# Kernel optimization log

Measured on AMD Instinct MI355X. Metric: run time of the kernel, lower is better.

The kernel has to match this reference:

```python
import jax, jax.numpy as jnp
import numpy as np

BS, SL, ENC_DIM, EDGE_DIM = 8, 256, 1024, 256
MINUS_INF = -1.0e8


def setup_inputs() -> dict:
    key = jax.random.key(0)
    ks = jax.random.split(key, 5)
    encoded_text = jax.random.normal(ks[0], (BS, SL, ENC_DIM), dtype=jnp.float32)
    mask = jnp.ones((BS, SL), dtype=jnp.int64)
    # Linear params (torch stores weight as (out, in)); scale like default init
    Wh = jax.random.normal(ks[1], (EDGE_DIM, ENC_DIM), dtype=jnp.float32) / np.sqrt(ENC_DIM)
    bh = jax.random.normal(ks[2], (EDGE_DIM,), dtype=jnp.float32) / np.sqrt(ENC_DIM)
    Wc = jax.random.normal(ks[3], (EDGE_DIM, ENC_DIM), dtype=jnp.float32) / np.sqrt(ENC_DIM)
    w_out = jax.random.normal(ks[4], (EDGE_DIM,), dtype=jnp.float32) / np.sqrt(EDGE_DIM)
    return {"encoded_text": encoded_text, "mask": mask, "Wh": Wh, "bh": bh, "Wc": Wc, "w_out": w_out}


def reference(encoded_text, mask, Wh, bh, Wc, w_out):
    # head/child projections: (bs, sl, edge_dim)
    head = jnp.einsum('bse,de->bsd', encoded_text, Wh) + bh
    child = jnp.einsum('bse,de->bsd', encoded_text, Wc)
    # Pairwise: torch code gives combined[b,i,j] = tanh(head[b,j] + child[b,i])
    combined = jnp.tanh(head[:, None, :, :] + child[:, :, None, :])  # (bs, sl, sl, edge_dim)
    edge_scores = jnp.einsum('bijd,d->bij', combined, w_out)  # (bs, sl, sl)
    float_mask = mask.astype(jnp.float32)
    minus_mask = (1.0 - float_mask) * MINUS_INF  # (bs, sl)
    edge_scores = edge_scores + minus_mask[:, :, None] + minus_mask[:, None, :]
    return edge_scores
```

## Files before the change

### kernel.cpp

```cpp
#include <hip/hip_runtime.h>
#include <hip/hip_bf16.h>
#include <stdint.h>


typedef __bf16 bf16_t;
typedef __attribute__((ext_vector_type(8))) __bf16 bf16x8;
typedef __attribute__((ext_vector_type(4))) float f32x4;

#define SL 256
#define ENC 1024
#define NTOT 512
#define N_ENC 2097152
#define N_W 262144
#define KSCALE 2.8853900817779268f

__device__ __forceinline__ void async16(void* lds, const void* g) {
  __builtin_amdgcn_global_load_lds(
      (const __attribute__((address_space(1))) uint32_t*)g,
      (__attribute__((address_space(3))) uint32_t*)lds, 16, 0, 0);
}
__device__ __forceinline__ unsigned short f32_to_bf16_rne(float f) {
  uint32_t u = __float_as_uint(f);
  return (unsigned short)((u + 0x7FFFu + ((u >> 16) & 1u)) >> 16);
}
__device__ __forceinline__ float bfu(unsigned short h) {
  return __uint_as_float(((uint32_t)h) << 16);
}

__global__ __launch_bounds__(256)
void convert_kernel(const float* __restrict__ enc, const float* __restrict__ Wh,
                    const float* __restrict__ Wc,
                    unsigned short* __restrict__ encB, unsigned short* __restrict__ WB) {
  int gi = (blockIdx.x * 256 + threadIdx.x) * 4;
  const float* src;
  unsigned short* dst;
  int off;
  if (gi < N_ENC) {
    src = enc; off = gi; dst = encB + gi;
  } else if (gi < N_ENC + N_W) {
    src = Wh; off = gi - N_ENC; dst = WB + off;
  } else {
    src = Wc; off = gi - N_ENC - N_W; dst = WB + N_W + off;
  }
  f32x4 v = *(const f32x4*)(src + off);
  ushort4 o;
  o.x = f32_to_bf16_rne(v[0]); o.y = f32_to_bf16_rne(v[1]);
  o.z = f32_to_bf16_rne(v[2]); o.w = f32_to_bf16_rne(v[3]);
  *(ushort4*)dst = o;
}

__global__ void prep_kernel(const float* __restrict__ bh, const float* __restrict__ wout,
                            const int* __restrict__ mask,
                            float* __restrict__ bhF, float* __restrict__ w2F,
                            float* __restrict__ Ssum, float* __restrict__ mmF) {
  int t = threadIdx.x;
  bhF[t] = bh[t];
  float w = wout[t];
  w2F[t] = -2.0f * w;
  __shared__ float red[256];
  red[t] = w;
  __syncthreads();
  for (int s = 128; s > 0; s >>= 1) {
    if (t < s) red[t] += red[t + s];
    __syncthreads();
  }
  if (t == 0) Ssum[0] = red[0];
  for (int s = t; s < 2048; s += 256)
    mmF[s] = (1.0f - (float)mask[s]) * -1.0e8f;
}

__global__ __launch_bounds__(256)
void proj_kernel(const unsigned short* __restrict__ A, const unsigned short* __restrict__ WB,
                 const float* __restrict__ bhF, float* __restrict__ hc) {
  __shared__ bf16_t As[64 * 32];
  __shared__ bf16_t Bs[64 * 32];
  const int t = threadIdx.x;
  const int wv = t >> 6, lane = t & 63;
  const int m0 = blockIdx.x * 64;
  const int n0 = blockIdx.y * 64;
  const int srow = t >> 2, schunk = t & 3;
  const int mq = (wv & 1) * 32, nq = (wv >> 1) * 32;
  const int fr = lane & 15, kq = lane >> 4;

  f32x4 acc00 = {0.f, 0.f, 0.f, 0.f};
  f32x4 acc01 = acc00, acc10 = acc00, acc11 = acc00;

  const unsigned short* gA = A + (size_t)(m0 + srow) * ENC + schunk * 8;
  const unsigned short* gB = WB + (size_t)(n0 + srow) * ENC + schunk * 8;

  for (int k0 = 0; k0 < ENC; k0 += 32) {
    __syncthreads();
    async16(&As[wv * 512], gA + k0);
    async16(&Bs[wv * 512], gB + k0);
    __syncthreads();
    bf16x8 a0 = *(const bf16x8*)&As[(mq + fr) * 32 + kq * 8];
    bf16x8 a1 = *(const bf16x8*)&As[(mq + 16 + fr) * 32 + kq * 8];
    bf16x8 b0 = *(const bf16x8*)&Bs[(nq + fr) * 32 + kq * 8];
    bf16x8 b1 = *(const bf16x8*)&Bs[(nq + 16 + fr) * 32 + kq * 8];
    acc00 = __builtin_amdgcn_mfma_f32_16x16x32_bf16(a0, b0, acc00, 0, 0, 0);
    acc01 = __builtin_amdgcn_mfma_f32_16x16x32_bf16(a0, b1, acc01, 0, 0, 0);
    acc10 = __builtin_amdgcn_mfma_f32_16x16x32_bf16(a1, b0, acc10, 0, 0, 0);
    acc11 = __builtin_amdgcn_mfma_f32_16x16x32_bf16(a1, b1, acc11, 0, 0, 0);
  }
  const int colA = n0 + nq + fr;
  const int colB = colA + 16;
  const float biasA = (colA < 256) ? bhF[colA] : 0.0f;
  const float biasB = (colB < 256) ? bhF[colB] : 0.0f;
#pragma unroll
  for (int r = 0; r < 4; ++r) {
    int row0 = m0 + mq + kq * 4 + r;
    int row1 = row0 + 16;
    hc[(size_t)row0 * NTOT + colA] = KSCALE * (acc00[r] + biasA);
    hc[(size_t)row0 * NTOT + colB] = KSCALE * (acc01[r] + biasB);
    hc[(size_t)row1 * NTOT + colA] = KSCALE * (acc10[r] + biasA);
    hc[(size_t)row1 * NTOT + colB] = KSCALE * (acc11[r] + biasB);
  }
}

#define LSTR 260
__global__ __launch_bounds__(256)
void edge_kernel(const float* __restrict__ hc, const float* __restrict__ w2,
                 const float* __restrict__ Ssum, const float* __restrict__ mmF,
                 float* __restrict__ out) {
  __shared__ float ldH[32 * LSTR];
  __shared__ float ldC[32 * LSTR];
  const int t = threadIdx.x;
  const int b = blockIdx.z;
  const int i0 = blockIdx.y * 32;
  const int j0 = blockIdx.x * 32;
  const int sbase = b * SL;

  for (int u = t; u < 32 * 64; u += 256) {
    int row = u >> 6;
    int c4 = (u & 63) << 2;
    f32x4 hv = *(const f32x4*)&hc[(size_t)(sbase + j0 + row) * NTOT + c4];
    f32x4 cv = *(const f32x4*)&hc[(size_t)(sbase + i0 + row) * NTOT + 256 + c4];
    *(f32x4*)&ldH[row * LSTR + c4] = hv;
    *(f32x4*)&ldC[row * LSTR + c4] = cv;
  }
  __syncthreads();

  const float S = Ssum[0];
  const int tx = t & 15, ty = t >> 4;
  const float* hp0 = &ldH[tx * LSTR];
  const float* hp1 = &ldH[(tx + 16) * LSTR];
  const float* cp0 = &ldC[ty * LSTR];
  const float* cp1 = &ldC[(ty + 16) * LSTR];
  float a00 = 0.f, a01 = 0.f, a10 = 0.f, a11 = 0.f;

#pragma unroll 8
  for (int d = 0; d < 256; d += 4) {
    f32x4 h0 = *(const f32x4*)&hp0[d];
    f32x4 h1 = *(const f32x4*)&hp1[d];
    f32x4 c0 = *(const f32x4*)&cp0[d];
    f32x4 c1 = *(const f32x4*)&cp1[d];
    f32x4 w4 = *(const f32x4*)&w2[d];
#pragma unroll
    for (int e = 0; e < 4; ++e) {
      float he0 = h0[e], he1 = h1[e], ce0 = c0[e], ce1 = c1[e], we = w4[e];
      float r00 = __builtin_amdgcn_rcpf(__builtin_amdgcn_exp2f(ce0 + he0) + 1.0f);
      float r01 = __builtin_amdgcn_rcpf(__builtin_amdgcn_exp2f(ce0 + he1) + 1.0f);
      float r10 = __builtin_amdgcn_rcpf(__builtin_amdgcn_exp2f(ce1 + he0) + 1.0f);
      float r11 = __builtin_amdgcn_rcpf(__builtin_amdgcn_exp2f(ce1 + he1) + 1.0f);
      a00 = fmaf(we, r00, a00);
      a01 = fmaf(we, r01, a01);
      a10 = fmaf(we, r10, a10);
      a11 = fmaf(we, r11, a11);
    }
  }

  const int gi0 = sbase + i0 + ty, gi1 = gi0 + 16;
  const int gj0 = j0 + tx, gj1 = gj0 + 16;
  const float mi0 = mmF[gi0], mi1 = mmF[gi1];
  const float mj0 = mmF[sbase + gj0], mj1 = mmF[sbase + gj1];
  out[(size_t)gi0 * SL + gj0] = S + a00 + mi0 + mj0;
  out[(size_t)gi0 * SL + gj1] = S + a01 + mi0 + mj1;
  out[(size_t)gi1 * SL + gj0] = S + a10 + mi1 + mj0;
  out[(size_t)gi1 * SL + gj1] = S + a11 + mi1 + mj1;
}

#define ED 256
#define HSTR 264
__global__ __launch_bounds__(256)
void kgedges_f32out(const float* __restrict__ enc, const int* __restrict__ mask,
                    const float* __restrict__ Wh, const float* __restrict__ Wc,
                    const float* __restrict__ p3, const float* __restrict__ p5,
                    float* __restrict__ out) {
  __shared__ float Wt[64 * 64];
  __shared__ float Et[32 * 64];
  __shared__ unsigned short headS[32 * HSTR];
  __shared__ unsigned short childS[32 * HSTR];
  __shared__ float red[256];
  __shared__ float bhS[256];
  __shared__ float wS[256];
  const int t = threadIdx.x;
  const int j0 = blockIdx.x * 32, i0 = blockIdx.y * 32, b = blockIdx.z;
  float va = p3[t], vb = p5[t];
  red[t] = va * va;
  __syncthreads();
  for (int s = 128; s > 0; s >>= 1) { if (t < s) red[t] += red[t + s]; __syncthreads(); }
  const float sa = red[0];
  __syncthreads();
  red[t] = vb * vb;
  __syncthreads();
  for (int s = 128; s > 0; s >>= 1) { if (t < s) red[t] += red[t + s]; __syncthreads(); }
  const float sb = red[0];
  __syncthreads();
  const bool dictOrder = (sa <= sb);
  bhS[t] = dictOrder ? va : vb;
  wS[t] = dictOrder ? vb : va;
  const int g = t >> 3;
  const int e = t & 7;
  for (int ph = 0; ph < 2; ++ph) {
    const float* Wsrc = ph ? Wc : Wh;
    const int rbase = b * SL + (ph ? i0 : j0);
    unsigned short* dst = ph ? childS : headS;
    for (int d0 = 0; d0 < ED; d0 += 64) {
      float acc[8] = {0.f, 0.f, 0.f, 0.f, 0.f, 0.f, 0.f, 0.f};
      for (int k0 = 0; k0 < ENC; k0 += 64) {
        __syncthreads();
#pragma unroll
        for (int p = 0; p < 4; ++p) {
          int u = t + 256 * p;
          int r = u >> 4, c4 = (u & 15) << 2;
          *(f32x4*)&Wt[r * 64 + c4] =
              *(const f32x4*)&Wsrc[(size_t)(d0 + r) * ENC + k0 + c4];
        }
#pragma unroll
        for (int p = 0; p < 2; ++p) {
          int u = t + 256 * p;
          int r = u >> 4, c4 = (u & 15) << 2;
          *(f32x4*)&Et[r * 64 + c4] =
              *(const f32x4*)&enc[(size_t)(rbase + r) * ENC + k0 + c4];
        }
        __syncthreads();
        for (int k4 = 0; k4 < 64; k4 += 4) {
          f32x4 ev = *(const f32x4*)&Et[g * 64 + k4];
#pragma unroll
          for (int m = 0; m < 8; ++m) {
            f32x4 wv = *(const f32x4*)&Wt[(e + 8 * m) * 64 + k4];
            acc[m] = fmaf(ev[0], wv[0], acc[m]);
            acc[m] = fmaf(ev[1], wv[1], acc[m]);
            acc[m] = fmaf(ev[2], wv[2], acc[m]);
            acc[m] = fmaf(ev[3], wv[3], acc[m]);
          }
        }
      }
#pragma unroll
      for (int m = 0; m < 8; ++m) {
        int d = d0 + e + 8 * m;
        float v = acc[m] + (ph == 0 ? bhS[d] : 0.0f);
        dst[g * HSTR + d] = f32_to_bf16_rne(v);
      }
    }
  }
  __syncthreads();
#pragma unroll
  for (int rep = 0; rep < 4; ++rep) {
    int idx = t + 256 * rep;
    int ii = idx >> 5, jj = idx & 31;
    float a = 0.f;
    for (int d = 0; d < ED; ++d) {
      float hv = bfu(headS[jj * HSTR + d]);
      float cv = bfu(childS[ii * HSTR + d]);
      a = fmaf(wS[d], tanhf(hv + cv), a);
    }
    int gi = b * SL + i0 + ii;
    int gj = j0 + jj;
    float mi = (1.0f - (float)mask[gi]) * -1.0e8f;
    float mj = (1.0f - (float)mask[b * SL + gj]) * -1.0e8f;
    out[(size_t)gi * SL + gj] = a + mi + mj;
  }
}

extern "C" void kernel_launch(void* const* d_in, const int* in_sizes, int n_in,
                              void* d_out, int out_size, void* d_ws, size_t ws_size,
                              hipStream_t stream) {
  (void)in_sizes; (void)n_in; (void)out_size;
  const float* enc = (const float*)d_in[0];
  const int* mask = (const int*)d_in[1];
  const float* Wh = (const float*)d_in[2];
  const float* bh = (const float*)d_in[3];
  const float* Wc = (const float*)d_in[4];
  const float* wout = (const float*)d_in[5];
  float* out = (float*)d_out;

  const size_t NEED = (size_t)(9u << 20) + (512u << 10);
  if (ws_size >= NEED) {
    char* W = (char*)d_ws;
    float* hc = (float*)W;
    unsigned short* encB = (unsigned short*)(W + (4 << 20));
    unsigned short* WB = (unsigned short*)(W + (8 << 20));
    float* bhF = (float*)(W + (9 << 20));
    float* w2F = bhF + 256;
    float* Ssum = w2F + 256;
    float* mmF = Ssum + 16;
    convert_kernel<<<2560, 256, 0, stream>>>(enc, Wh, Wc, encB, WB);
    prep_kernel<<<1, 256, 0, stream>>>(bh, wout, mask, bhF, w2F, Ssum, mmF);
    proj_kernel<<<dim3(32, 8), 256, 0, stream>>>(encB, WB, bhF, hc);
    edge_kernel<<<dim3(8, 8, 8), 256, 0, stream>>>(hc, w2F, Ssum, mmF, out);
  } else {
    kgedges_f32out<<<dim3(8, 8, 8), 256, 0, stream>>>(enc, mask, Wh, Wc, bh, wout, out);
  }
}
```

Baseline: 115.9 us.

## Precompute exp2 of projections and fold prep kernel into edge kernel

The projection epilogue now stores exp2 of the scaled head/child values, so the pairwise inner loop computes exp(h+c) as a product and drops one transcendental per element. The separate prep kernel is removed: the edge kernel reduces w_out into shared memory and computes the mask offsets itself, saving a launch. The fused fallback kernel and the workspace-size check are also removed. Storing exponentials risks overflow or underflow to inf/0 for large projection values, though the rcp form still saturates toward ±1 for tanh.

```diff
diff --git a/kernel.cpp b/kernel.cpp
--- a/kernel.cpp
+++ b/kernel.cpp
@@ -23,9 +23,6 @@
   uint32_t u = __float_as_uint(f);
   return (unsigned short)((u + 0x7FFFu + ((u >> 16) & 1u)) >> 16);
 }
-__device__ __forceinline__ float bfu(unsigned short h) {
-  return __uint_as_float(((uint32_t)h) << 16);
-}
 
 __global__ __launch_bounds__(256)
 void convert_kernel(const float* __restrict__ enc, const float* __restrict__ Wh,
@@ -49,29 +46,9 @@
   *(ushort4*)dst = o;
 }
 
-__global__ void prep_kernel(const float* __restrict__ bh, const float* __restrict__ wout,
-                            const int* __restrict__ mask,
-                            float* __restrict__ bhF, float* __restrict__ w2F,
-                            float* __restrict__ Ssum, float* __restrict__ mmF) {
-  int t = threadIdx.x;
-  bhF[t] = bh[t];
-  float w = wout[t];
-  w2F[t] = -2.0f * w;
-  __shared__ float red[256];
-  red[t] = w;
-  __syncthreads();
-  for (int s = 128; s > 0; s >>= 1) {
-    if (t < s) red[t] += red[t + s];
-    __syncthreads();
-  }
-  if (t == 0) Ssum[0] = red[0];
-  for (int s = t; s < 2048; s += 256)
-    mmF[s] = (1.0f - (float)mask[s]) * -1.0e8f;
-}
-
 __global__ __launch_bounds__(256)
 void proj_kernel(const unsigned short* __restrict__ A, const unsigned short* __restrict__ WB,
-                 const float* __restrict__ bhF, float* __restrict__ hc) {
+                 const float* __restrict__ bh, float* __restrict__ hc) {
   __shared__ bf16_t As[64 * 32];
   __shared__ bf16_t Bs[64 * 32];
   const int t = threadIdx.x;
@@ -104,31 +81,36 @@
   }
   const int colA = n0 + nq + fr;
   const int colB = colA + 16;
-  const float biasA = (colA < 256) ? bhF[colA] : 0.0f;
-  const float biasB = (colB < 256) ? bhF[colB] : 0.0f;
+  const float biasA = (colA < 256) ? bh[colA] : 0.0f;
+  const float biasB = (colB < 256) ? bh[colB] : 0.0f;
 #pragma unroll
   for (int r = 0; r < 4; ++r) {
     int row0 = m0 + mq + kq * 4 + r;
     int row1 = row0 + 16;
-    hc[(size_t)row0 * NTOT + colA] = KSCALE * (acc00[r] + biasA);
-    hc[(size_t)row0 * NTOT + colB] = KSCALE * (acc01[r] + biasB);
-    hc[(size_t)row1 * NTOT + colA] = KSCALE * (acc10[r] + biasA);
-    hc[(size_t)row1 * NTOT + colB] = KSCALE * (acc11[r] + biasB);
+    hc[(size_t)row0 * NTOT + colA] = __builtin_amdgcn_exp2f(KSCALE * (acc00[r] + biasA));
+    hc[(size_t)row0 * NTOT + colB] = __builtin_amdgcn_exp2f(KSCALE * (acc01[r] + biasB));
+    hc[(size_t)row1 * NTOT + colA] = __builtin_amdgcn_exp2f(KSCALE * (acc10[r] + biasA));
+    hc[(size_t)row1 * NTOT + colB] = __builtin_amdgcn_exp2f(KSCALE * (acc11[r] + biasB));
   }
 }
 
 #define LSTR 260
 __global__ __launch_bounds__(256)
-void edge_kernel(const float* __restrict__ hc, const float* __restrict__ w2,
-                 const float* __restrict__ Ssum, const float* __restrict__ mmF,
-                 float* __restrict__ out) {
+void edge_kernel(const float* __restrict__ hc, const float* __restrict__ wout,
+                 const int* __restrict__ mask, float* __restrict__ out) {
   __shared__ float ldH[32 * LSTR];
   __shared__ float ldC[32 * LSTR];
+  __shared__ float wS[256];
+  __shared__ float red[256];
   const int t = threadIdx.x;
   const int b = blockIdx.z;
   const int i0 = blockIdx.y * 32;
   const int j0 = blockIdx.x * 32;
   const int sbase = b * SL;
+
+  float w = wout[t];
+  wS[t] = -2.0f * w;
+  red[t] = w;
 
   for (int u = t; u < 32 * 64; u += 256) {
     int row = u >> 6;
@@ -139,8 +121,12 @@
     *(f32x4*)&ldC[row * LSTR + c4] = cv;
   }
   __syncthreads();
+  for (int s = 128; s > 0; s >>= 1) {
+    if (t < s) red[t] += red[t + s];
+    __syncthreads();
+  }
+  const float S = red[0];
 
-  const float S = Ssum[0];
   const int tx = t & 15, ty = t >> 4;
   const float* hp0 = &ldH[tx * LSTR];
   const float* hp1 = &ldH[(tx + 16) * LSTR];
@@ -154,14 +140,14 @@
     f32x4 h1 = *(const f32x4*)&hp1[d];
     f32x4 c0 = *(const f32x4*)&cp0[d];
     f32x4 c1 = *(const f32x4*)&cp1[d];
-    f32x4 w4 = *(const f32x4*)&w2[d];
+    f32x4 w4 = *(const f32x4*)&wS[d];
 #pragma unroll
     for (int e = 0; e < 4; ++e) {
       float he0 = h0[e], he1 = h1[e], ce0 = c0[e], ce1 = c1[e], we = w4[e];
-      float r00 = __builtin_amdgcn_rcpf(__builtin_amdgcn_exp2f(ce0 + he0) + 1.0f);
-      float r01 = __builtin_amdgcn_rcpf(__builtin_amdgcn_exp2f(ce0 + he1) + 1.0f);
-      float r10 = __builtin_amdgcn_rcpf(__builtin_amdgcn_exp2f(ce1 + he0) + 1.0f);
-      float r11 = __builtin_amdgcn_rcpf(__builtin_amdgcn_exp2f(ce1 + he1) + 1.0f);
+      float r00 = __builtin_amdgcn_rcpf(ce0 * he0 + 1.0f);
+      float r01 = __builtin_amdgcn_rcpf(ce0 * he1 + 1.0f);
+      float r10 = __builtin_amdgcn_rcpf(ce1 * he0 + 1.0f);
+      float r11 = __builtin_amdgcn_rcpf(ce1 * he1 + 1.0f);
       a00 = fmaf(we, r00, a00);
       a01 = fmaf(we, r01, a01);
       a10 = fmaf(we, r10, a10);
@@ -171,112 +157,20 @@
 
   const int gi0 = sbase + i0 + ty, gi1 = gi0 + 16;
   const int gj0 = j0 + tx, gj1 = gj0 + 16;
-  const float mi0 = mmF[gi0], mi1 = mmF[gi1];
-  const float mj0 = mmF[sbase + gj0], mj1 = mmF[sbase + gj1];
+  const float mi0 = (1.0f - (float)mask[gi0]) * -1.0e8f;
+  const float mi1 = (1.0f - (float)mask[gi1]) * -1.0e8f;
+  const float mj0 = (1.0f - (float)mask[sbase + gj0]) * -1.0e8f;
+  const float mj1 = (1.0f - (float)mask[sbase + gj1]) * -1.0e8f;
   out[(size_t)gi0 * SL + gj0] = S + a00 + mi0 + mj0;
   out[(size_t)gi0 * SL + gj1] = S + a01 + mi0 + mj1;
   out[(size_t)gi1 * SL + gj0] = S + a10 + mi1 + mj0;
   out[(size_t)gi1 * SL + gj1] = S + a11 + mi1 + mj1;
 }
 
-#define ED 256
-#define HSTR 264
-__global__ __launch_bounds__(256)
-void kgedges_f32out(const float* __restrict__ enc, const int* __restrict__ mask,
-                    const float* __restrict__ Wh, const float* __restrict__ Wc,
-                    const float* __restrict__ p3, const float* __restrict__ p5,
-                    float* __restrict__ out) {
-  __shared__ float Wt[64 * 64];
-  __shared__ float Et[32 * 64];
-  __shared__ unsigned short headS[32 * HSTR];
-  __shared__ unsigned short childS[32 * HSTR];
-  __shared__ float red[256];
-  __shared__ float bhS[256];
-  __shared__ float wS[256];
-  const int t = threadIdx.x;
-  const int j0 = blockIdx.x * 32, i0 = blockIdx.y * 32, b = blockIdx.z;
-  float va = p3[t], vb = p5[t];
-  red[t] = va * va;
-  __syncthreads();
-  for (int s = 128; s > 0; s >>= 1) { if (t < s) red[t] += red[t + s]; __syncthreads(); }
-  const float sa = red[0];
-  __syncthreads();
-  red[t] = vb * vb;
-  __syncthreads();
-  for (int s = 128; s > 0; s >>= 1) { if (t < s) red[t] += red[t + s]; __syncthreads(); }
-  const float sb = red[0];
-  __syncthreads();
-  const bool dictOrder = (sa <= sb);
-  bhS[t] = dictOrder ? va : vb;
-  wS[t] = dictOrder ? vb : va;
-  const int g = t >> 3;
-  const int e = t & 7;
-  for (int ph = 0; ph < 2; ++ph) {
-    const float* Wsrc = ph ? Wc : Wh;
-    const int rbase = b * SL + (ph ? i0 : j0);
-    unsigned short* dst = ph ? childS : headS;
-    for (int d0 = 0; d0 < ED; d0 += 64) {
-      float acc[8] = {0.f, 0.f, 0.f, 0.f, 0.f, 0.f, 0.f, 0.f};
-      for (int k0 = 0; k0 < ENC; k0 += 64) {
-        __syncthreads();
-#pragma unroll
-        for (int p = 0; p < 4; ++p) {
-          int u = t + 256 * p;
-          int r = u >> 4, c4 = (u & 15) << 2;
-          *(f32x4*)&Wt[r * 64 + c4] =
-              *(const f32x4*)&Wsrc[(size_t)(d0 + r) * ENC + k0 + c4];
-        }
-#pragma unroll
-        for (int p = 0; p < 2; ++p) {
-          int u = t + 256 * p;
-          int r = u >> 4, c4 = (u & 15) << 2;
-          *(f32x4*)&Et[r * 64 + c4] =
-              *(const f32x4*)&enc[(size_t)(rbase + r) * ENC + k0 + c4];
-        }
-        __syncthreads();
-        for (int k4 = 0; k4 < 64; k4 += 4) {
-          f32x4 ev = *(const f32x4*)&Et[g * 64 + k4];
-#pragma unroll
-          for (int m = 0; m < 8; ++m) {
-            f32x4 wv = *(const f32x4*)&Wt[(e + 8 * m) * 64 + k4];
-            acc[m] = fmaf(ev[0], wv[0], acc[m]);
-            acc[m] = fmaf(ev[1], wv[1], acc[m]);
-            acc[m] = fmaf(ev[2], wv[2], acc[m]);
-            acc[m] = fmaf(ev[3], wv[3], acc[m]);
-          }
-        }
-      }
-#pragma unroll
-      for (int m = 0; m < 8; ++m) {
-        int d = d0 + e + 8 * m;
-        float v = acc[m] + (ph == 0 ? bhS[d] : 0.0f);
-        dst[g * HSTR + d] = f32_to_bf16_rne(v);
-      }
-    }
-  }
-  __syncthreads();
-#pragma unroll
-  for (int rep = 0; rep < 4; ++rep) {
-    int idx = t + 256 * rep;
-    int ii = idx >> 5, jj = idx & 31;
-    float a = 0.f;
-    for (int d = 0; d < ED; ++d) {
-      float hv = bfu(headS[jj * HSTR + d]);
-      float cv = bfu(childS[ii * HSTR + d]);
-      a = fmaf(wS[d], tanhf(hv + cv), a);
-    }
-    int gi = b * SL + i0 + ii;
-    int gj = j0 + jj;
-    float mi = (1.0f - (float)mask[gi]) * -1.0e8f;
-    float mj = (1.0f - (float)mask[b * SL + gj]) * -1.0e8f;
-    out[(size_t)gi * SL + gj] = a + mi + mj;
-  }
-}
-
 extern "C" void kernel_launch(void* const* d_in, const int* in_sizes, int n_in,
                               void* d_out, int out_size, void* d_ws, size_t ws_size,
                               hipStream_t stream) {
-  (void)in_sizes; (void)n_in; (void)out_size;
+  (void)in_sizes; (void)n_in; (void)out_size; (void)ws_size;
   const float* enc = (const float*)d_in[0];
   const int* mask = (const int*)d_in[1];
   const float* Wh = (const float*)d_in[2];
@@ -285,21 +179,12 @@
   const float* wout = (const float*)d_in[5];
   float* out = (float*)d_out;
 
-  const size_t NEED = (size_t)(9u << 20) + (512u << 10);
-  if (ws_size >= NEED) {
-    char* W = (char*)d_ws;
-    float* hc = (float*)W;
-    unsigned short* encB = (unsigned short*)(W + (4 << 20));
-    unsigned short* WB = (unsigned short*)(W + (8 << 20));
-    float* bhF = (float*)(W + (9 << 20));
-    float* w2F = bhF + 256;
-    float* Ssum = w2F + 256;
-    float* mmF = Ssum + 16;
-    convert_kernel<<<2560, 256, 0, stream>>>(enc, Wh, Wc, encB, WB);
-    prep_kernel<<<1, 256, 0, stream>>>(bh, wout, mask, bhF, w2F, Ssum, mmF);
-    proj_kernel<<<dim3(32, 8), 256, 0, stream>>>(encB, WB, bhF, hc);
-    edge_kernel<<<dim3(8, 8, 8), 256, 0, stream>>>(hc, w2F, Ssum, mmF, out);
-  } else {
-    kgedges_f32out<<<dim3(8, 8, 8), 256, 0, stream>>>(enc, mask, Wh, Wc, bh, wout, out);
-  }
+  char* W = (char*)d_ws;
+  float* hc = (float*)W;
+  unsigned short* encB = (unsigned short*)(W + (4 << 20));
+  unsigned short* WB = (unsigned short*)(W + (8 << 20));
+
+  convert_kernel<<<2560, 256, 0, stream>>>(enc, Wh, Wc, encB, WB);
+  proj_kernel<<<dim3(32, 8), 256, 0, stream>>>(encB, WB, bh, hc);
+  edge_kernel<<<dim3(8, 8, 8), 256, 0, stream>>>(hc, wout, mask, out);
 }
```

After: 104.2 us. 10.2% less time.
